# Optimization experiments

Hardware: AMD Instinct MI355X
Metric: run time of the kernel (lower is better)

The kernel has to match this reference:

```python
import jax, jax.numpy as jnp
import numpy as np

DIM = 512
HEADS = 8
DIM_HEAD = DIM // 8          # 64
INNER = HEADS * DIM_HEAD     # 512
M_LANDMARKS = DIM // 2       # 256
PINV_ITERS = 6
RES_KERNEL = 33
LN_EPS = 1e-5


def setup_inputs() -> dict:
    key = jax.random.key(0)
    ks = jax.random.split(key, 7)
    b, n = 8, 4096
    x = jax.random.normal(ks[0], (b, n, DIM), dtype=jnp.float32)
    gamma = jnp.ones((DIM,), jnp.float32)
    beta = jnp.zeros((DIM,), jnp.float32)
    w_qkv = jax.random.normal(ks[1], (DIM, 3 * INNER), jnp.float32) * 0.02
    w_out = jax.random.normal(ks[2], (INNER, DIM), jnp.float32) * 0.02
    b_out = jnp.zeros((DIM,), jnp.float32)
    # depthwise Conv2d(heads, heads, (33,1), groups=heads): torch weight [H,1,33,1]
    res_kernel = jax.random.normal(ks[3], (HEADS, 1, RES_KERNEL, 1), jnp.float32) * 0.05
    return {"x": x, "gamma": gamma, "beta": beta, "w_qkv": w_qkv,
            "w_out": w_out, "b_out": b_out, "res_kernel": res_kernel}


def _moore_penrose_pinv(a, iters=PINV_ITERS):
    # a: [b, h, m, m]
    abs_a = jnp.abs(a)
    col = abs_a.sum(axis=-1).max()   # global max, as in torch.max(col)
    row = abs_a.sum(axis=-2).max()
    z = jnp.swapaxes(a, -1, -2) / (col * row)
    I = jnp.eye(a.shape[-1], dtype=a.dtype)
    for _ in range(iters):
        az = a @ z
        z = 0.25 * z @ (13. * I - az @ (15. * I - az @ (7. * I - az)))
    return z


def _nystrom_attention(xn, w_qkv, res_kernel, w_out, b_out):
    b, n, _ = xn.shape
    h, dh, m = HEADS, DIM_HEAD, M_LANDMARKS
    scale = dh ** -0.5
    qkv = xn @ w_qkv                               # [b, n, 3*inner]
    q, k, v = jnp.split(qkv, 3, axis=-1)
    def to_heads(t):
        return t.reshape(b, n, h, dh).transpose(0, 2, 1, 3)  # [b,h,n,dh]
    q, k, v = to_heads(q), to_heads(k), to_heads(v)
    q = q * scale

    l = n // m  # n chosen as multiple of m -> no padding branch
    # landmark pooling: '(m l) d -> m d' mean
    q_l = q.reshape(b, h, m, l, dh).mean(axis=3)   # [b,h,m,dh]
    k_l = k.reshape(b, h, m, l, dh).mean(axis=3)

    sim1 = jnp.einsum('bhid,bhjd->bhij', q, k_l)    # [b,h,n,m]
    sim2 = jnp.einsum('bhid,bhjd->bhij', q_l, k_l)  # [b,h,m,m]
    sim3 = jnp.einsum('bhid,bhjd->bhij', q_l, k)    # [b,h,m,n]

    attn1 = jax.nn.softmax(sim1, axis=-1)
    attn2 = jax.nn.softmax(sim2, axis=-1)
    attn3 = jax.nn.softmax(sim3, axis=-1)

    attn2_inv = _moore_penrose_pinv(attn2)
    out = (attn1 @ attn2_inv) @ (attn3 @ v)         # [b,h,n,dh]

    # residual depthwise conv over sequence dim (kernel 33x1, groups=heads)
    pad = RES_KERNEL // 2
    out = out + jax.lax.conv_general_dilated(
        v, res_kernel, window_strides=(1, 1),
        padding=((pad, pad), (0, 0)),
        dimension_numbers=('NCHW', 'OIHW', 'NCHW'),
        feature_group_count=HEADS)

    out = out.transpose(0, 2, 1, 3).reshape(b, n, h * dh)  # [b,n,inner]
    return out @ w_out + b_out  # dropout omitted (eval mode)


def reference(x, gamma, beta, w_qkv, w_out, b_out, res_kernel):
    mu = x.mean(axis=-1, keepdims=True)
    var = x.var(axis=-1, keepdims=True)
    xn = (x - mu) * jax.lax.rsqrt(var + LN_EPS) * gamma + beta
    return x + _nystrom_attention(xn, w_qkv, res_kernel, w_out, b_out)
```

## Files before the change

### kernel.cpp

```cpp
#include <hip/hip_runtime.h>

#define SEQ 4096
#define DMODEL 512
#define NH 8
#define DH 64
#define MLM 256
#define NBH 64
#define NROWS 32768

typedef unsigned short bf16_t;
typedef __attribute__((ext_vector_type(8))) short bf16x8;
typedef __attribute__((ext_vector_type(4))) float f32x4;

__device__ __forceinline__ float bf2f(unsigned short u) {
  return __uint_as_float(((unsigned)u) << 16);
}
__device__ __forceinline__ unsigned short f2bf(float f) {
  unsigned u = __float_as_uint(f);
  u += 0x7fffu + ((u >> 16) & 1u);
  return (unsigned short)(u >> 16);
}
__device__ __forceinline__ void unp8(const bf16_t* p, float* d) {
  uint4 u = *(const uint4*)p;
  d[0] = __uint_as_float(u.x << 16); d[1] = __uint_as_float(u.x & 0xffff0000u);
  d[2] = __uint_as_float(u.y << 16); d[3] = __uint_as_float(u.y & 0xffff0000u);
  d[4] = __uint_as_float(u.z << 16); d[5] = __uint_as_float(u.z & 0xffff0000u);
  d[6] = __uint_as_float(u.w << 16); d[7] = __uint_as_float(u.w & 0xffff0000u);
}

__device__ __forceinline__ void gll16(const void* g, void* l) {
  __builtin_amdgcn_global_load_lds(
      (const __attribute__((address_space(1))) unsigned int*)g,
      (__attribute__((address_space(3))) unsigned int*)l, 16, 0, 0);
}

__global__ __launch_bounds__(64) void ln_kernel(const float* __restrict__ x,
    const float* __restrict__ gamma, const float* __restrict__ beta,
    bf16_t* __restrict__ xn) {
  int row = blockIdx.x;
  const float4* xr = (const float4*)(x + (size_t)row * DMODEL);
  int t = threadIdx.x;
  float4 a = xr[t], b = xr[t + 64];
  float s  = a.x + a.y + a.z + a.w + b.x + b.y + b.z + b.w;
  float ss = a.x*a.x + a.y*a.y + a.z*a.z + a.w*a.w
           + b.x*b.x + b.y*b.y + b.z*b.z + b.w*b.w;
#pragma unroll
  for (int off = 32; off > 0; off >>= 1) {
    s  += __shfl_xor(s, off);
    ss += __shfl_xor(ss, off);
  }
  float mean = s * (1.0f / DMODEL);
  float var  = ss * (1.0f / DMODEL) - mean * mean;
  float rstd = rsqrtf(var + 1e-5f);
  const float4* g4 = (const float4*)gamma;
  const float4* be4 = (const float4*)beta;
  ushort4* o = (ushort4*)(xn + (size_t)row * DMODEL);
  float4 g = g4[t], bb = be4[t];
  ushort4 r;
  r.x = f2bf((a.x - mean) * rstd * g.x + bb.x);
  r.y = f2bf((a.y - mean) * rstd * g.y + bb.y);
  r.z = f2bf((a.z - mean) * rstd * g.z + bb.z);
  r.w = f2bf((a.w - mean) * rstd * g.w + bb.w);
  o[t] = r;
  g = g4[t + 64]; bb = be4[t + 64];
  r.x = f2bf((b.x - mean) * rstd * g.x + bb.x);
  r.y = f2bf((b.y - mean) * rstd * g.y + bb.y);
  r.z = f2bf((b.z - mean) * rstd * g.z + bb.z);
  r.w = f2bf((b.w - mean) * rstd * g.w + bb.w);
  o[t + 64] = r;
}

__global__ __launch_bounds__(256) void convT(const float* __restrict__ w,
    bf16_t* __restrict__ wt, int K, int N) {
  size_t idx = (size_t)blockIdx.x * 256 + threadIdx.x;
  int n = (int)(idx / K), k = (int)(idx % K);
  wt[idx] = f2bf(w[(size_t)k * N + n]);
}

#define MFMA_GEMM_BODY(APTR, BTPTR, KDIM) \
  __shared__ short As[128][32]; \
  __shared__ short Bs[128][32]; \
  int tid = threadIdx.x; \
  int lane = tid & 63; \
  int wv = tid >> 6; \
  int wm = (wv & 1) << 6, wn = (wv >> 1) << 6; \
  int l15 = lane & 15, l16 = lane >> 4; \
  f32x4 acc[4][4]; \
  _Pragma("unroll") for (int fm = 0; fm < 4; ++fm) \
    _Pragma("unroll") for (int fn = 0; fn < 4; ++fn) \
      acc[fm][fn] = (f32x4){0.f, 0.f, 0.f, 0.f}; \
  int ar0 = tid >> 2, ac0 = (tid & 3) << 3; \
  const bf16_t* Ab  = (APTR) + (size_t)(m0 + ar0) * (KDIM) + ac0; \
  const bf16_t* Ab1 = (APTR) + (size_t)(m0 + ar0 + 64) * (KDIM) + ac0; \
  const bf16_t* Bb  = (BTPTR) + (size_t)(n0 + ar0) * (KDIM) + ac0; \
  const bf16_t* Bb1 = (BTPTR) + (size_t)(n0 + ar0 + 64) * (KDIM) + ac0; \
  short* AsW  = &As[(wv << 4)][0]; \
  short* AsW1 = &As[64 + (wv << 4)][0]; \
  short* BsW  = &Bs[(wv << 4)][0]; \
  short* BsW1 = &Bs[64 + (wv << 4)][0]; \
  for (int k0 = 0; k0 < (KDIM); k0 += 32) { \
    gll16(Ab + k0, AsW);  gll16(Ab1 + k0, AsW1); \
    gll16(Bb + k0, BsW);  gll16(Bb1 + k0, BsW1); \
    __syncthreads(); \
    bf16x8 af[4], bfr[4]; \
    _Pragma("unroll") for (int f = 0; f < 4; ++f) { \
      af[f]  = *(const bf16x8*)&As[wm + f * 16 + l15][l16 * 8]; \
      bfr[f] = *(const bf16x8*)&Bs[wn + f * 16 + l15][l16 * 8]; \
    } \
    _Pragma("unroll") for (int fm = 0; fm < 4; ++fm) \
      _Pragma("unroll") for (int fn = 0; fn < 4; ++fn) \
        acc[fm][fn] = __builtin_amdgcn_mfma_f32_16x16x32_bf16(af[fm], bfr[fn], acc[fm][fn], 0, 0, 0); \
    __syncthreads(); \
  }

__global__ __launch_bounds__(256) void gemm_qkv_mfma(const bf16_t* __restrict__ A,
    const bf16_t* __restrict__ BT, bf16_t* __restrict__ q, bf16_t* __restrict__ k,
    bf16_t* __restrict__ v, bf16_t* __restrict__ vT) {
  int bid = blockIdx.x;
  int orig = (bid & 7) * 384 + (bid >> 3);
  int n0 = (orig % 12) << 7;
  int m0 = (orig / 12) << 7;
  MFMA_GEMM_BODY(A, BT, 512)
#pragma unroll
  for (int fm = 0; fm < 4; ++fm) {
    int row0 = m0 + wm + fm * 16 + l16 * 4;
    int bat = row0 >> 12;
    int nn0 = row0 & 4095;
#pragma unroll
    for (int fn = 0; fn < 4; ++fn) {
      int col = n0 + wn + fn * 16 + l15;
      int which = col >> 9;
      int hd = (col >> 6) & 7;
      int d  = col & 63;
      if (which == 2) {
        ushort4 pk;
        pk.x = f2bf(acc[fm][fn][0]); pk.y = f2bf(acc[fm][fn][1]);
        pk.z = f2bf(acc[fm][fn][2]); pk.w = f2bf(acc[fm][fn][3]);
        *(ushort4*)(vT + ((size_t)(bat * NH + hd) * DH + d) * SEQ + nn0) = pk;
#pragma unroll
        for (int rg = 0; rg < 4; ++rg)
          v[(((size_t)(bat * NH + hd)) * SEQ + nn0 + rg) * DH + d] = f2bf(acc[fm][fn][rg]);
      } else {
        bf16_t* dst = (which == 0) ? q : k;
        float scale = (which == 0) ? 0.125f : 1.f;
#pragma unroll
        for (int rg = 0; rg < 4; ++rg)
          dst[(((size_t)(bat * NH + hd)) * SEQ + nn0 + rg) * DH + d] = f2bf(acc[fm][fn][rg] * scale);
      }
    }
  }
}

__global__ __launch_bounds__(256) void gemm_out_mfma(const bf16_t* __restrict__ A,
    const bf16_t* __restrict__ BT, const float* __restrict__ bias,
    const float* __restrict__ x, float* __restrict__ y) {
  int bid = blockIdx.x;
  int orig = (bid & 7) * 128 + (bid >> 3);
  int n0 = (orig & 3) << 7;
  int m0 = (orig >> 2) << 7;
  MFMA_GEMM_BODY(A, BT, 512)
#pragma unroll
  for (int fm = 0; fm < 4; ++fm) {
#pragma unroll
    for (int fn = 0; fn < 4; ++fn) {
      int col = n0 + wn + fn * 16 + l15;
      float bv = bias[col];
#pragma unroll
      for (int rg = 0; rg < 4; ++rg) {
        int row = m0 + wm + fm * 16 + l16 * 4 + rg;
        y[(size_t)row * DMODEL + col] = x[(size_t)row * DMODEL + col] + acc[fm][fn][rg] + bv;
      }
    }
  }
}

__global__ __launch_bounds__(256) void bmm_mfma32(const bf16_t* __restrict__ Ag,
    const bf16_t* __restrict__ BTg, bf16_t* __restrict__ Cb,
    bf16_t* __restrict__ CTb, float* __restrict__ Cf,
    int K, float alpha, float eA, float diagc, int flags) {
  int bid = blockIdx.x;
  int orig = (bid & 7) * 512 + (bid >> 3);
  int bh = orig >> 6;
  int tile = orig & 63;
  int n0 = (tile & 7) << 5;
  int m0 = (tile >> 3) << 5;
  const bf16_t* A  = Ag + (size_t)bh * 256 * K;
  const bf16_t* BT = BTg + (size_t)bh * 256 * K;
  __shared__ short As[32][36];
  __shared__ short Bs[32][36];
  int tid = threadIdx.x;
  int lane = tid & 63;
  int wv = tid >> 6;
  int wm = (wv & 1) << 4, wn = (wv >> 1) << 4;
  int l15 = lane & 15, l16 = lane >> 4;
  f32x4 acc = (f32x4){0.f, 0.f, 0.f, 0.f};
  int ar0 = tid >> 3, ac0 = (tid & 7) << 2;
  const bf16_t* Ab = A + (size_t)(m0 + ar0) * K + ac0;
  const bf16_t* Bb = BT + (size_t)(n0 + ar0) * K + ac0;
  uint2 ga = *(const uint2*)Ab;
  uint2 gb = *(const uint2*)Bb;
  for (int k0 = 0; k0 < K; k0 += 32) {
    *(uint2*)&As[ar0][ac0] = ga;
    *(uint2*)&Bs[ar0][ac0] = gb;
    __syncthreads();
    if (k0 + 32 < K) {
      ga = *(const uint2*)(Ab + k0 + 32);
      gb = *(const uint2*)(Bb + k0 + 32);
    }
    bf16x8 af = *(const bf16x8*)&As[wm + l15][l16 * 8];
    bf16x8 bf = *(const bf16x8*)&Bs[wn + l15][l16 * 8];
    acc = __builtin_amdgcn_mfma_f32_16x16x32_bf16(af, bf, acc, 0, 0, 0);
    __syncthreads();
  }
  size_t cbase = (size_t)bh * 65536;
  int row0 = m0 + wm + l16 * 4;
  int col = n0 + wn + l15;
  float v4[4];
#pragma unroll
  for (int rg = 0; rg < 4; ++rg) {
    float val = alpha * acc[rg];
    if (eA != 0.f) val += eA * bf2f(A[(size_t)(row0 + rg) * K + col]);
    if (row0 + rg == col) val += diagc;
    v4[rg] = val;
  }
  if (flags & 1) {
#pragma unroll
    for (int rg = 0; rg < 4; ++rg)
      Cb[cbase + (size_t)(row0 + rg) * 256 + col] = f2bf(v4[rg]);
  }
  if (flags & 2) {
    ushort4 pk;
    pk.x = f2bf(v4[0]); pk.y = f2bf(v4[1]);
    pk.z = f2bf(v4[2]); pk.w = f2bf(v4[3]);
    *(ushort4*)(CTb + cbase + (size_t)col * 256 + row0) = pk;
  }
  if (flags & 4) {
#pragma unroll
    for (int rg = 0; rg < 4; ++rg)
      Cf[cbase + (size_t)(row0 + rg) * 256 + col] = v4[rg];
  }
}

__global__ __launch_bounds__(256) void ns_zy32(const bf16_t* __restrict__ zg,
    const bf16_t* __restrict__ Yg, const bf16_t* __restrict__ t1Tg,
    bf16_t* __restrict__ zog, bf16_t* __restrict__ Yog,
    bf16_t* __restrict__ YTog) {
  int bid = blockIdx.x;
  int orig = (bid & 7) * 1024 + (bid >> 3);
  int task = orig >> 6;
  int bh = task >> 1;
  int which = task & 1;
  int tile = orig & 63;
  int n0 = (tile & 7) << 5;
  int m0 = (tile >> 3) << 5;
  const bf16_t* A  = (which ? Yg : zg) + ((size_t)bh << 16);
  const bf16_t* BT = t1Tg + ((size_t)bh << 16);
  __shared__ short As[32][36];
  __shared__ short Bs[32][36];
  int tid = threadIdx.x;
  int lane = tid & 63;
  int wv = tid >> 6;
  int wm = (wv & 1) << 4, wn = (wv >> 1) << 4;
  int l15 = lane & 15, l16 = lane >> 4;
  f32x4 acc = (f32x4){0.f, 0.f, 0.f, 0.f};
  int ar0 = tid >> 3, ac0 = (tid & 7) << 2;
  const bf16_t* Ab = A + (size_t)(m0 + ar0) * 256 + ac0;
  const bf16_t* Bb = BT + (size_t)(n0 + ar0) * 256 + ac0;
  uint2 ga = *(const uint2*)Ab;
  uint2 gb = *(const uint2*)Bb;
  for (int k0 = 0; k0 < 256; k0 += 32) {
    *(uint2*)&As[ar0][ac0] = ga;
    *(uint2*)&Bs[ar0][ac0] = gb;
    __syncthreads();
    if (k0 + 32 < 256) {
      ga = *(const uint2*)(Ab + k0 + 32);
      gb = *(const uint2*)(Bb + k0 + 32);
    }
    bf16x8 af = *(const bf16x8*)&As[wm + l15][l16 * 8];
    bf16x8 bf = *(const bf16x8*)&Bs[wn + l15][l16 * 8];
    acc = __builtin_amdgcn_mfma_f32_16x16x32_bf16(af, bf, acc, 0, 0, 0);
    __syncthreads();
  }
  size_t cbase = (size_t)bh << 16;
  int row0 = m0 + wm + l16 * 4;
  int col = n0 + wn + l15;
  float v4[4];
#pragma unroll
  for (int rg = 0; rg < 4; ++rg) v4[rg] = 0.25f * acc[rg];
  if (which == 0) {
#pragma unroll
    for (int rg = 0; rg < 4; ++rg)
      zog[cbase + (size_t)(row0 + rg) * 256 + col] = f2bf(v4[rg]);
  } else {
#pragma unroll
    for (int rg = 0; rg < 4; ++rg)
      Yog[cbase + (size_t)(row0 + rg) * 256 + col] = f2bf(v4[rg]);
    ushort4 pk;
    pk.x = f2bf(v4[0]); pk.y = f2bf(v4[1]);
    pk.z = f2bf(v4[2]); pk.w = f2bf(v4[3]);
    *(ushort4*)(YTog + cbase + (size_t)col * 256 + row0) = pk;
  }
}

__global__ __launch_bounds__(64) void pool_kernel(const bf16_t* __restrict__ q,
    const bf16_t* __restrict__ k, bf16_t* __restrict__ qlb,
    bf16_t* __restrict__ klb) {
  int bh = blockIdx.y, i = blockIdx.x, d = threadIdx.x;
  const bf16_t* qb = q + ((size_t)bh * SEQ + i * 16) * DH + d;
  const bf16_t* kb = k + ((size_t)bh * SEQ + i * 16) * DH + d;
  float sq = 0.f, sk = 0.f;
#pragma unroll
  for (int j = 0; j < 16; ++j) { sq += bf2f(qb[j * DH]); sk += bf2f(kb[j * DH]); }
  sq *= (1.f / 16.f); sk *= (1.f / 16.f);
  qlb[((size_t)bh * MLM + i) * DH + d] = f2bf(sq);
  klb[((size_t)bh * MLM + i) * DH + d] = f2bf(sk);
}

__global__ __launch_bounds__(256) void softmax256(const float* __restrict__ af,
    bf16_t* __restrict__ ab) {
  const float* ar = af + (size_t)blockIdx.x * MLM;
  int t = threadIdx.x;
  float v = ar[t];
  __shared__ float redm[4], reds[4];
  float m = v;
#pragma unroll
  for (int off = 32; off > 0; off >>= 1) m = fmaxf(m, __shfl_xor(m, off));
  if ((t & 63) == 0) redm[t >> 6] = m;
  __syncthreads();
  m = fmaxf(fmaxf(redm[0], redm[1]), fmaxf(redm[2], redm[3]));
  float p = __expf(v - m);
  float s = p;
#pragma unroll
  for (int off = 32; off > 0; off >>= 1) s += __shfl_xor(s, off);
  if ((t & 63) == 0) reds[t >> 6] = s;
  __syncthreads();
  s = reds[0] + reds[1] + reds[2] + reds[3];
  ab[(size_t)blockIdx.x * MLM + t] = f2bf(p / s);
}

__global__ void init_scal(unsigned* s) { if (threadIdx.x < 2) s[threadIdx.x] = 0u; }

__global__ __launch_bounds__(256) void colrow_max(const bf16_t* __restrict__ a,
    unsigned* __restrict__ scal) {
  int bh = blockIdx.x;
  int task = blockIdx.y;
  const bf16_t* ab = a + (size_t)bh * MLM * MLM;
  int t = threadIdx.x;
  float s = 0.f;
  if (task == 0) {
    const bf16_t* rp = ab + (size_t)t * MLM;
    for (int j = 0; j < MLM; j += 8) {
      float d[8];
      unp8(rp + j, d);
      s += d[0]; s += d[1]; s += d[2]; s += d[3];
      s += d[4]; s += d[5]; s += d[6]; s += d[7];
    }
  } else {
    for (int i = 0; i < MLM; ++i) s += bf2f(ab[(size_t)i * MLM + t]);
  }
  __shared__ float red[4];
  float m = s;
#pragma unroll
  for (int off = 32; off > 0; off >>= 1) m = fmaxf(m, __shfl_xor(m, off));
  if ((t & 63) == 0) red[t >> 6] = m;
  __syncthreads();
  if (t == 0) {
    m = fmaxf(fmaxf(red[0], red[1]), fmaxf(red[2], red[3]));
    atomicMax(scal + task, __float_as_uint(m));
  }
}

__global__ __launch_bounds__(256) void zinit(const bf16_t* __restrict__ ab,
    bf16_t* __restrict__ z0, bf16_t* __restrict__ z0T,
    const unsigned* __restrict__ scal) {
  size_t idx = (size_t)blockIdx.x * 256 + threadIdx.x;
  float denom = __uint_as_float(scal[0]) * __uint_as_float(scal[1]);
  size_t bh = idx >> 16;
  int i = (int)((idx >> 8) & 255);
  int j = (int)(idx & 255);
  bf16_t r = f2bf(bf2f(ab[idx]) / denom);
  z0T[idx] = r;
  z0[(bh << 16) + ((size_t)j << 8) + i] = r;
}

__global__ __launch_bounds__(64) void attn3v_mfma(const bf16_t* __restrict__ qlb,
    const bf16_t* __restrict__ kg, const bf16_t* __restrict__ vT,
    float* __restrict__ pacc, float* __restrict__ pm, float* __restrict__ ps) {
  int bid = blockIdx.x;
  int orig = (bid & 7) * 512 + (bid >> 3);
  int m0 = (orig & 7) << 5;
  int cz = (orig >> 3) & 7;
  int bh = orig >> 6;
  int lane = threadIdx.x;
  int l15 = lane & 15, l16 = lane >> 4;
  __shared__ short plds[32][136];
  const bf16_t* qbase = qlb + (size_t)bh * MLM * DH;
  const bf16_t* kbase = kg + (size_t)bh * SEQ * DH;
  const bf16_t* vbase = vT + (size_t)bh * DH * SEQ;
  bf16x8 af[2][2];
#pragma unroll
  for (int mt = 0; mt < 2; ++mt)
#pragma unroll
    for (int ks = 0; ks < 2; ++ks)
      af[mt][ks] = *(const bf16x8*)(qbase + (size_t)(m0 + mt * 16 + l15) * DH + ks * 32 + l16 * 8);
  float m_run[2][4], s_run[2][4];
  f32x4 o[2][4];
#pragma unroll
  for (int mt = 0; mt < 2; ++mt) {
#pragma unroll
    for (int rg = 0; rg < 4; ++rg) { m_run[mt][rg] = -1e30f; s_run[mt][rg] = 0.f; }
#pragma unroll
    for (int n2 = 0; n2 < 4; ++n2) o[mt][n2] = (f32x4){0.f, 0.f, 0.f, 0.f};
  }
  int kbeg = cz << 9;
  for (int kt = kbeg; kt < kbeg + 512; kt += 128) {
    f32x4 sacc[2][8];
#pragma unroll
    for (int mt = 0; mt < 2; ++mt)
#pragma unroll
      for (int nt = 0; nt < 8; ++nt) sacc[mt][nt] = (f32x4){0.f, 0.f, 0.f, 0.f};
#pragma unroll
    for (int nt = 0; nt < 8; ++nt) {
      const bf16_t* kr = kbase + (size_t)(kt + nt * 16 + l15) * DH + l16 * 8;
      bf16x8 b0 = *(const bf16x8*)kr;
      bf16x8 b1 = *(const bf16x8*)(kr + 32);
      sacc[0][nt] = __builtin_amdgcn_mfma_f32_16x16x32_bf16(af[0][0], b0, sacc[0][nt], 0, 0, 0);
      sacc[0][nt] = __builtin_amdgcn_mfma_f32_16x16x32_bf16(af[0][1], b1, sacc[0][nt], 0, 0, 0);
      sacc[1][nt] = __builtin_amdgcn_mfma_f32_16x16x32_bf16(af[1][0], b0, sacc[1][nt], 0, 0, 0);
      sacc[1][nt] = __builtin_amdgcn_mfma_f32_16x16x32_bf16(af[1][1], b1, sacc[1][nt], 0, 0, 0);
    }
#pragma unroll
    for (int mt = 0; mt < 2; ++mt)
#pragma unroll
      for (int rg = 0; rg < 4; ++rg) {
        float mx = sacc[mt][0][rg];
#pragma unroll
        for (int nt = 1; nt < 8; ++nt) mx = fmaxf(mx, sacc[mt][nt][rg]);
        mx = fmaxf(mx, __shfl_xor(mx, 1));
        mx = fmaxf(mx, __shfl_xor(mx, 2));
        mx = fmaxf(mx, __shfl_xor(mx, 4));
        mx = fmaxf(mx, __shfl_xor(mx, 8));
        float mnew = fmaxf(m_run[mt][rg], mx);
        float corr = __expf(m_run[mt][rg] - mnew);
        float s = 0.f;
#pragma unroll
        for (int nt = 0; nt < 8; ++nt) {
          float p = __expf(sacc[mt][nt][rg] - mnew);
          sacc[mt][nt][rg] = p;
          s += p;
        }
        s += __shfl_xor(s, 1); s += __shfl_xor(s, 2);
        s += __shfl_xor(s, 4); s += __shfl_xor(s, 8);
        s_run[mt][rg] = s_run[mt][rg] * corr + s;
        m_run[mt][rg] = mnew;
#pragma unroll
        for (int n2 = 0; n2 < 4; ++n2) o[mt][n2][rg] *= corr;
      }
#pragma unroll
    for (int mt = 0; mt < 2; ++mt)
#pragma unroll
      for (int nt = 0; nt < 8; ++nt)
#pragma unroll
        for (int rg = 0; rg < 4; ++rg)
          plds[mt * 16 + l16 * 4 + rg][nt * 16 + l15] = (short)f2bf(sacc[mt][nt][rg]);
#pragma unroll
    for (int ks2 = 0; ks2 < 4; ++ks2) {
      bf16x8 pa0 = *(const bf16x8*)&plds[l15][ks2 * 32 + l16 * 8];
      bf16x8 pa1 = *(const bf16x8*)&plds[16 + l15][ks2 * 32 + l16 * 8];
#pragma unroll
      for (int n2 = 0; n2 < 4; ++n2) {
        bf16x8 vb8 = *(const bf16x8*)(vbase + (size_t)(n2 * 16 + l15) * SEQ + kt + ks2 * 32 + l16 * 8);
        o[0][n2] = __builtin_amdgcn_mfma_f32_16x16x32_bf16(pa0, vb8, o[0][n2], 0, 0, 0);
        o[1][n2] = __builtin_amdgcn_mfma_f32_16x16x32_bf16(pa1, vb8, o[1][n2], 0, 0, 0);
      }
    }
  }
  size_t pidx0 = (size_t)(bh * 8 + cz) * MLM + m0;
#pragma unroll
  for (int mt = 0; mt < 2; ++mt)
#pragma unroll
    for (int n2 = 0; n2 < 4; ++n2)
#pragma unroll
      for (int rg = 0; rg < 4; ++rg) {
        int row = mt * 16 + l16 * 4 + rg;
        pacc[(pidx0 + row) * 64 + n2 * 16 + l15] = o[mt][n2][rg];
      }
  if (l15 == 0) {
#pragma unroll
    for (int mt = 0; mt < 2; ++mt)
#pragma unroll
      for (int rg = 0; rg < 4; ++rg) {
        pm[pidx0 + mt * 16 + l16 * 4 + rg] = m_run[mt][rg];
        ps[pidx0 + mt * 16 + l16 * 4 + rg] = s_run[mt][rg];
      }
  }
}

__global__ __launch_bounds__(256) void attn3v_comb(const float* __restrict__ pacc,
    const float* __restrict__ pm, const float* __restrict__ ps,
    bf16_t* __restrict__ a3vb) {
  int gw = blockIdx.x * 4 + (threadIdx.x >> 6);
  int lane = threadIdx.x & 63;
  int bh = gw >> 8, row = gw & 255;
  float ms[8];
  float M = -1e30f;
#pragma unroll
  for (int cc = 0; cc < 8; ++cc) {
    ms[cc] = pm[(size_t)(bh * 8 + cc) * MLM + row];
    M = fmaxf(M, ms[cc]);
  }
  float S = 0.f, val = 0.f;
#pragma unroll
  for (int cc = 0; cc < 8; ++cc) {
    size_t pidx = (size_t)(bh * 8 + cc) * MLM + row;
    float w = __expf(ms[cc] - M);
    S += w * ps[pidx];
    val += w * pacc[pidx * 64 + lane];
  }
  a3vb[(size_t)gw * 64 + lane] = f2bf(val / S);
}

__global__ __launch_bounds__(256) void wm_kernel(const bf16_t* __restrict__ zb,
    const bf16_t* __restrict__ a3vb, bf16_t* __restrict__ wmT) {
  int bh = blockIdx.y;
  int m0 = blockIdx.x << 6;
  __shared__ bf16_t a3s[MLM * DH];
  int t = threadIdx.x;
  const bf16_t* asrc = a3vb + (size_t)bh * MLM * DH;
#pragma unroll
  for (int i = 0; i < 8; ++i)
    *(bf16x8*)(a3s + ((size_t)t + 256 * i) * 8) =
        *(const bf16x8*)(asrc + ((size_t)t + 256 * i) * 8);
  __syncthreads();
  int row = m0 + (t >> 2);
  int c0 = (t & 3) * 16;
  const bf16_t* zrow = zb + (size_t)bh * 65536 + (size_t)row * 256;
  float acc16[16] = {};
  for (int k0 = 0; k0 < 256; k0 += 8) {
    float a8[8];
    unp8(zrow + k0, a8);
#pragma unroll
    for (int j = 0; j < 8; ++j) {
      float av[16];
      unp8(a3s + (k0 + j) * 64 + c0, av);
      unp8(a3s + (k0 + j) * 64 + c0 + 8, av + 8);
#pragma unroll
      for (int e = 0; e < 16; ++e) acc16[e] += a8[j] * av[e];
    }
  }
  bf16_t* wd = wmT + (size_t)bh * DH * MLM;
#pragma unroll
  for (int e = 0; e < 16; ++e)
    wd[(size_t)(c0 + e) * MLM + row] = f2bf(acc16[e]);
}

__global__ __launch_bounds__(64) void attn1_mfma(const bf16_t* __restrict__ qg,
    const bf16_t* __restrict__ klb, const bf16_t* __restrict__ wmT,
    bf16_t* __restrict__ om) {
  int bh = blockIdx.y, bat = bh >> 3, head = bh & 7;
  int m0 = blockIdx.x << 5;
  int lane = threadIdx.x;
  int l15 = lane & 15, l16 = lane >> 4;
  __shared__ short plds[32][264];
  const bf16_t* qbase = qg + (size_t)bh * SEQ * DH;
  const bf16_t* kbase = klb + (size_t)bh * MLM * DH;
  bf16x8 af[2][2];
#pragma unroll
  for (int mt = 0; mt < 2; ++mt)
#pragma unroll
    for (int ks = 0; ks < 2; ++ks)
      af[mt][ks] = *(const bf16x8*)(qbase + (size_t)(m0 + mt * 16 + l15) * DH + ks * 32 + l16 * 8);
  f32x4 acc[2][16];
#pragma unroll
  for (int mt = 0; mt < 2; ++mt)
#pragma unroll
    for (int nt = 0; nt < 16; ++nt) acc[mt][nt] = (f32x4){0.f, 0.f, 0.f, 0.f};
#pragma unroll
  for (int nt = 0; nt < 16; ++nt) {
    bf16x8 b0 = *(const bf16x8*)(kbase + (size_t)(nt * 16 + l15) * DH + l16 * 8);
    bf16x8 b1 = *(const bf16x8*)(kbase + (size_t)(nt * 16 + l15) * DH + 32 + l16 * 8);
    acc[0][nt] = __builtin_amdgcn_mfma_f32_16x16x32_bf16(af[0][0], b0, acc[0][nt], 0, 0, 0);
    acc[0][nt] = __builtin_amdgcn_mfma_f32_16x16x32_bf16(af[0][1], b1, acc[0][nt], 0, 0, 0);
    acc[1][nt] = __builtin_amdgcn_mfma_f32_16x16x32_bf16(af[1][0], b0, acc[1][nt], 0, 0, 0);
    acc[1][nt] = __builtin_amdgcn_mfma_f32_16x16x32_bf16(af[1][1], b1, acc[1][nt], 0, 0, 0);
  }
  float inv[2][4];
#pragma unroll
  for (int mt = 0; mt < 2; ++mt)
#pragma unroll
    for (int rg = 0; rg < 4; ++rg) {
      float mx = acc[mt][0][rg];
#pragma unroll
      for (int nt = 1; nt < 16; ++nt) mx = fmaxf(mx, acc[mt][nt][rg]);
      mx = fmaxf(mx, __shfl_xor(mx, 1));
      mx = fmaxf(mx, __shfl_xor(mx, 2));
      mx = fmaxf(mx, __shfl_xor(mx, 4));
      mx = fmaxf(mx, __shfl_xor(mx, 8));
      float s = 0.f;
#pragma unroll
      for (int nt = 0; nt < 16; ++nt) {
        float p = __expf(acc[mt][nt][rg] - mx);
        acc[mt][nt][rg] = p;
        s += p;
      }
      s += __shfl_xor(s, 1); s += __shfl_xor(s, 2);
      s += __shfl_xor(s, 4); s += __shfl_xor(s, 8);
      inv[mt][rg] = 1.f / s;
    }
#pragma unroll
  for (int mt = 0; mt < 2; ++mt)
#pragma unroll
    for (int nt = 0; nt < 16; ++nt)
#pragma unroll
      for (int rg = 0; rg < 4; ++rg)
        plds[mt * 16 + l16 * 4 + rg][nt * 16 + l15] = (short)f2bf(acc[mt][nt][rg]);
  const bf16_t* wbase = wmT + (size_t)bh * DH * MLM;
  f32x4 o[2][4];
#pragma unroll
  for (int mt = 0; mt < 2; ++mt)
#pragma unroll
    for (int n2 = 0; n2 < 4; ++n2) o[mt][n2] = (f32x4){0.f, 0.f, 0.f, 0.f};
#pragma unroll
  for (int ks = 0; ks < 8; ++ks) {
    bf16x8 pa0 = *(const bf16x8*)&plds[l15][ks * 32 + l16 * 8];
    bf16x8 pa1 = *(const bf16x8*)&plds[16 + l15][ks * 32 + l16 * 8];
#pragma unroll
    for (int n2 = 0; n2 < 4; ++n2) {
      bf16x8 wb = *(const bf16x8*)(wbase + (size_t)(n2 * 16 + l15) * MLM + ks * 32 + l16 * 8);
      o[0][n2] = __builtin_amdgcn_mfma_f32_16x16x32_bf16(pa0, wb, o[0][n2], 0, 0, 0);
      o[1][n2] = __builtin_amdgcn_mfma_f32_16x16x32_bf16(pa1, wb, o[1][n2], 0, 0, 0);
    }
  }
#pragma unroll
  for (int mt = 0; mt < 2; ++mt)
#pragma unroll
    for (int n2 = 0; n2 < 4; ++n2)
#pragma unroll
      for (int rg = 0; rg < 4; ++rg) {
        int n = m0 + mt * 16 + l16 * 4 + rg;
        int d = n2 * 16 + l15;
        om[((size_t)(bat * SEQ + n)) * DMODEL + head * DH + d] =
            f2bf(o[mt][n2][rg] * inv[mt][rg]);
      }
}

__global__ __launch_bounds__(256) void conv_add(const bf16_t* __restrict__ vg,
    const float* __restrict__ rk, bf16_t* __restrict__ om) {
  int bh = blockIdx.y, bat = bh >> 3, head = bh & 7;
  int n0 = blockIdx.x << 5;
  __shared__ bf16_t vs[64 * 64];
  int t = threadIdx.x;
  const bf16_t* vbase = vg + (size_t)bh * SEQ * DH;
#pragma unroll
  for (int i = 0; i < 2; ++i) {
    int li = t + 256 * i;
    int rr = li >> 3, cc = (li & 7) << 3;
    int src = n0 - 16 + rr;
    bf16x8 val;
    if (src >= 0 && src < SEQ) val = *(const bf16x8*)(vbase + (size_t)src * DH + cc);
    else { short z = 0; val = (bf16x8){z, z, z, z, z, z, z, z}; }
    *(bf16x8*)(vs + rr * 64 + cc) = val;
  }
  __syncthreads();
  float w[33];
#pragma unroll
  for (int i = 0; i < 33; ++i) w[i] = rk[head * 33 + i];
  int d = t & 63;
  int r0 = (t >> 6) << 3;
  float out[8] = {0.f, 0.f, 0.f, 0.f, 0.f, 0.f, 0.f, 0.f};
#pragma unroll
  for (int j = 0; j < 40; ++j) {
    float vv = bf2f(vs[(r0 + j) * 64 + d]);
    int ilo = j - 32; if (ilo < 0) ilo = 0;
    int ihi = j; if (ihi > 7) ihi = 7;
    for (int i = ilo; i <= ihi; ++i) out[i] += w[j - i] * vv;
  }
#pragma unroll
  for (int i = 0; i < 8; ++i) {
    int n = n0 + r0 + i;
    size_t idx = ((size_t)(bat * SEQ + n)) * DMODEL + head * DH + d;
    om[idx] = f2bf(bf2f(om[idx]) + out[i]);
  }
}

extern "C" void kernel_launch(void* const* d_in, const int* in_sizes, int n_in,
                              void* d_out, int out_size, void* d_ws, size_t ws_size,
                              hipStream_t stream) {
  const float* x     = (const float*)d_in[0];
  const float* gamma = (const float*)d_in[1];
  const float* beta  = (const float*)d_in[2];
  const float* w_qkv = (const float*)d_in[3];
  const float* w_out = (const float*)d_in[4];
  const float* b_out = (const float*)d_in[5];
  const float* rk    = (const float*)d_in[6];
  float* y  = (float*)d_out;

  bf16_t* xnb  = (bf16_t*)d_ws;
  bf16_t* qb   = xnb + 16777216;
  bf16_t* kb   = qb + 16777216;
  bf16_t* vb   = kb + 16777216;
  bf16_t* wqkvT = vb + 16777216;
  bf16_t* woutT = wqkvT + 786432;
  bf16_t* qlb  = woutT + 262144;
  bf16_t* klb  = qlb + 1048576;
  bf16_t* a2b  = klb + 1048576;
  bf16_t* zA   = a2b + 4194304;
  bf16_t* z0T  = zA + 4194304;
  bf16_t* zB   = z0T + 4194304;
  bf16_t* Ya   = zB + 4194304;
  bf16_t* Yb   = z0T;
  bf16_t* vTb  = zA;
  bf16_t* a3vb = Ya + 4194304;
  bf16_t* wmT  = a3vb + 1048576;
  float*  SR   = (float*)(wmT + 1048576);
  float*  a2f  = SR;
  float*  pacc = SR;
  bf16_t* YTa  = (bf16_t*)SR;
  bf16_t* YTb  = YTa + 4194304;
  bf16_t* t2T  = YTa + 8388608;
  bf16_t* t1T  = YTa + 12582912;
  float*  pm   = SR + 8388608;
  float*  ps   = pm + 131072;
  unsigned* scal = (unsigned*)(ps + 131072);
  size_t need = (size_t)93323264 * 2 + (size_t)(8388608 + 262144) * 4 + 64;
  if (ws_size < need) return;

  ln_kernel<<<NROWS, 64, 0, stream>>>(x, gamma, beta, xnb);
  convT<<<3072, 256, 0, stream>>>(w_qkv, wqkvT, 512, 1536);
  convT<<<1024, 256, 0, stream>>>(w_out, woutT, 512, 512);

  gemm_qkv_mfma<<<3072, 256, 0, stream>>>(xnb, wqkvT, qb, kb, vb, vTb);
  pool_kernel<<<dim3(MLM, NBH), 64, 0, stream>>>(qb, kb, qlb, klb);

  bmm_mfma32<<<4096, 256, 0, stream>>>(qlb, klb, nullptr, nullptr, a2f,
      64, 1.f, 0.f, 0.f, 4);
  softmax256<<<NBH * MLM, 256, 0, stream>>>(a2f, a2b);

  init_scal<<<1, 64, 0, stream>>>(scal);
  colrow_max<<<dim3(NBH, 2), 256, 0, stream>>>(a2b, scal);

  attn3v_mfma<<<4096, 64, 0, stream>>>(qlb, kb, vTb, pacc, pm, ps);
  attn3v_comb<<<4096, 256, 0, stream>>>(pacc, pm, ps, a3vb);

  zinit<<<16384, 256, 0, stream>>>(a2b, zA, z0T, scal);
  bmm_mfma32<<<4096, 256, 0, stream>>>(a2b, z0T, Ya, YTa, nullptr,
      256, 1.f, 0.f, 0.f, 3);
  bf16_t* zc = zA;  bf16_t* zo = zB;
  bf16_t* Yc = Ya;  bf16_t* YTc = YTa;
  bf16_t* Yo = Yb;  bf16_t* YTo = YTb;
  for (int it = 0; it < 6; ++it) {
    bmm_mfma32<<<4096, 256, 0, stream>>>(Yc, YTc, nullptr, t2T, nullptr,
        256, 1.f, -7.f, 15.f, 2);
    bmm_mfma32<<<4096, 256, 0, stream>>>(Yc, t2T, nullptr, t1T, nullptr,
        256, -1.f, 0.f, 13.f, 2);
    ns_zy32<<<8192, 256, 0, stream>>>(zc, Yc, t1T, zo, Yo, YTo);
    bf16_t* tp;
    tp = zc; zc = zo; zo = tp;
    tp = Yc; Yc = Yo; Yo = tp;
    tp = YTc; YTc = YTo; YTo = tp;
  }

  wm_kernel<<<dim3(4, NBH), 256, 0, stream>>>(zc, a3vb, wmT);

  bf16_t* om = xnb;
  attn1_mfma<<<dim3(SEQ / 32, NBH), 64, 0, stream>>>(qb, klb, wmT, om);
  conv_add<<<dim3(SEQ / 32, NBH), 256, 0, stream>>>(vb, rk, om);

  gemm_out_mfma<<<1024, 256, 0, stream>>>(om, woutT, b_out, x, y);
}
```

Measured before the change: 770.9 us.

## Rewrite QKV GEMM with 256x256 tiles, 4-stage LDS pipeline and swizzle

Replaces the 128x128 single-buffered QKV projection GEMM with a 256x256-tile, 512-thread kernel. It uses a 4-stage global_load_lds ring with explicit vmcnt waits, so loads for later k-steps overlap the MFMA work. LDS reads are XOR-swizzled to avoid bank conflicts, and s_setprio raises priority around the MFMA block. The larger tiles improve data reuse but raise register and LDS pressure (128 KB shared) and cut the grid to 768 blocks.

Result: no change. 766.9 us (-0.5%).

```diff
diff --git a/kernel.cpp b/kernel.cpp
--- a/kernel.cpp
+++ b/kernel.cpp
@@ -28,7 +28,7 @@
   d[6] = __uint_as_float(u.w << 16); d[7] = __uint_as_float(u.w & 0xffff0000u);
 }
 
-__device__ __forceinline__ void gll16(const void* g, void* l) {
+__device__ __forceinline__ void gll(const void* g, void* l) {
   __builtin_amdgcn_global_load_lds(
       (const __attribute__((address_space(1))) unsigned int*)g,
       (__attribute__((address_space(3))) unsigned int*)l, 16, 0, 0);
@@ -99,8 +99,8 @@
   short* BsW  = &Bs[(wv << 4)][0]; \
   short* BsW1 = &Bs[64 + (wv << 4)][0]; \
   for (int k0 = 0; k0 < (KDIM); k0 += 32) { \
-    gll16(Ab + k0, AsW);  gll16(Ab1 + k0, AsW1); \
-    gll16(Bb + k0, BsW);  gll16(Bb1 + k0, BsW1); \
+    gll(Ab + k0, AsW);  gll(Ab1 + k0, AsW1); \
+    gll(Bb + k0, BsW);  gll(Bb1 + k0, BsW1); \
     __syncthreads(); \
     bf16x8 af[4], bfr[4]; \
     _Pragma("unroll") for (int f = 0; f < 4; ++f) { \
@@ -113,22 +113,70 @@
     __syncthreads(); \
   }
 
-__global__ __launch_bounds__(256) void gemm_qkv_mfma(const bf16_t* __restrict__ A,
+__global__ __launch_bounds__(512) void gemm_qkv_256(const bf16_t* __restrict__ A,
     const bf16_t* __restrict__ BT, bf16_t* __restrict__ q, bf16_t* __restrict__ k,
     bf16_t* __restrict__ v, bf16_t* __restrict__ vT) {
   int bid = blockIdx.x;
-  int orig = (bid & 7) * 384 + (bid >> 3);
-  int n0 = (orig % 12) << 7;
-  int m0 = (orig / 12) << 7;
-  MFMA_GEMM_BODY(A, BT, 512)
-#pragma unroll
-  for (int fm = 0; fm < 4; ++fm) {
-    int row0 = m0 + wm + fm * 16 + l16 * 4;
+  int orig = (bid & 7) * 96 + (bid >> 3);
+  int n0 = (orig % 6) << 8;
+  int m0 = (orig / 6) << 8;
+  __shared__ short As[4][8192];
+  __shared__ short Bs[4][8192];
+  int tid = threadIdx.x;
+  int lane = tid & 63;
+  int wid = tid >> 6;
+  int wr = wid >> 2, wc = wid & 3;
+  int l15 = lane & 15, l16 = lane >> 4;
+  int sl = (l16 ^ (l15 & 3)) << 3;
+  int gr  = lane >> 2;
+  int gcs = ((lane & 3) ^ ((lane >> 2) & 3)) << 3;
+  f32x4 acc[8][4];
+#pragma unroll
+  for (int fm = 0; fm < 8; ++fm)
+#pragma unroll
+    for (int fn = 0; fn < 4; ++fn) acc[fm][fn] = (f32x4){0.f, 0.f, 0.f, 0.f};
+
+#define STAGE(kt, s) { \
+    _Pragma("unroll") for (int u = 0; u < 2; ++u) { \
+      int r0 = (wid << 5) + (u << 4); \
+      gll(A  + (size_t)(m0 + r0 + gr) * 512 + (kt) * 32 + gcs, &As[s][r0 << 5]); \
+      gll(BT + (size_t)(n0 + r0 + gr) * 512 + (kt) * 32 + gcs, &Bs[s][r0 << 5]); \
+    } }
+
+  STAGE(0, 0) STAGE(1, 1) STAGE(2, 2)
+  for (int t = 0; t < 16; ++t) {
+    int s = t & 3;
+    if (t < 14)       asm volatile("s_waitcnt vmcnt(8)" ::: "memory");
+    else if (t == 14) asm volatile("s_waitcnt vmcnt(4)" ::: "memory");
+    else              asm volatile("s_waitcnt vmcnt(0)" ::: "memory");
+    __builtin_amdgcn_s_barrier();
+    if (t + 3 < 16) STAGE(t + 3, ((t + 3) & 3))
+    bf16x8 a[8], b[4];
+#pragma unroll
+    for (int fm = 0; fm < 8; ++fm)
+      a[fm] = *(const bf16x8*)&As[s][(((wr << 7) + (fm << 4) + l15) << 5) + sl];
+#pragma unroll
+    for (int fn = 0; fn < 4; ++fn)
+      b[fn] = *(const bf16x8*)&Bs[s][(((wc << 6) + (fn << 4) + l15) << 5) + sl];
+    asm volatile("s_waitcnt lgkmcnt(0)" ::: "memory");
+    __builtin_amdgcn_sched_barrier(0);
+    __builtin_amdgcn_s_setprio(1);
+#pragma unroll
+    for (int fm = 0; fm < 8; ++fm)
+#pragma unroll
+      for (int fn = 0; fn < 4; ++fn)
+        acc[fm][fn] = __builtin_amdgcn_mfma_f32_16x16x32_bf16(a[fm], b[fn], acc[fm][fn], 0, 0, 0);
+    __builtin_amdgcn_s_setprio(0);
+  }
+#undef STAGE
+#pragma unroll
+  for (int fm = 0; fm < 8; ++fm) {
+    int row0 = m0 + (wr << 7) + (fm << 4) + (l16 << 2);
     int bat = row0 >> 12;
     int nn0 = row0 & 4095;
 #pragma unroll
     for (int fn = 0; fn < 4; ++fn) {
-      int col = n0 + wn + fn * 16 + l15;
+      int col = n0 + (wc << 6) + (fn << 4) + l15;
       int which = col >> 9;
       int hd = (col >> 6) & 7;
       int d  = col & 63;
@@ -729,7 +777,7 @@
   convT<<<3072, 256, 0, stream>>>(w_qkv, wqkvT, 512, 1536);
   convT<<<1024, 256, 0, stream>>>(w_out, woutT, 512, 512);
 
-  gemm_qkv_mfma<<<3072, 256, 0, stream>>>(xnb, wqkvT, qb, kb, vb, vTb);
+  gemm_qkv_256<<<768, 512, 0, stream>>>(xnb, wqkvT, qb, kb, vb, vTb);
   pool_kernel<<<dim3(MLM, NBH), 64, 0, stream>>>(qb, kb, qlb, klb);
 
   bmm_mfma32<<<4096, 256, 0, stream>>>(qlb, klb, nullptr, nullptr, a2f,
```
